# Kernel tuning notes

Hardware: AMD Instinct MI355X
Metric: run time of the kernel (lower is better)

The kernel has to match this reference:

```python
import jax, jax.numpy as jnp
import numpy as np
import math

H = 16        # num query heads
KV = 4        # num key/value heads
HD = 128      # head_dim
THETA = 10000.0

def _rope(x, cos, sin):
    # x: [B, h, S, HD]; cos/sin: [1, 1, S, HD//2]
    xr, xi = x[..., :HD // 2], x[..., HD // 2:]
    return jnp.concatenate([xr * cos - xi * sin, xr * sin + xi * cos], axis=-1)

def setup_inputs() -> dict:
    key = jax.random.key(0)
    ks = jax.random.split(key, 5)
    B, S, D = 1, 4096, 2048
    s = 1.0 / math.sqrt(D)
    return {
        "hidden_states": jax.random.normal(ks[0], (B, S, D), jnp.float32),
        "Wq": jax.random.normal(ks[1], (D, H * HD), jnp.float32) * s,
        "Wk": jax.random.normal(ks[2], (D, KV * HD), jnp.float32) * s,
        "Wv": jax.random.normal(ks[3], (D, KV * HD), jnp.float32) * s,
        "Wo": jax.random.normal(ks[4], (H * HD, D), jnp.float32) * s,
    }

def reference(hidden_states, Wq, Wk, Wv, Wo):
    B, S, D = hidden_states.shape
    # projections -> [B, h, S, HD]
    q = (hidden_states @ Wq).reshape(B, S, H, HD).transpose(0, 2, 1, 3)
    k = (hidden_states @ Wk).reshape(B, S, KV, HD).transpose(0, 2, 1, 3)
    v = (hidden_states @ Wv).reshape(B, S, KV, HD).transpose(0, 2, 1, 3)
    # rotary embedding (half-split layout, matching the torch module)
    inv_freq = 1.0 / (THETA ** (jnp.arange(0, HD, 2, dtype=jnp.float32) / HD))
    freqs = jnp.arange(S, dtype=jnp.float32)[:, None] * inv_freq[None, :]  # [S, HD//2]
    cos = jnp.cos(freqs)[None, None]
    sin = jnp.sin(freqs)[None, None]
    q = _rope(q, cos, sin)
    k = _rope(k, cos, sin)
    # GQA: repeat KV heads to match query heads
    rep = H // KV
    k = jnp.repeat(k, rep, axis=1)
    v = jnp.repeat(v, rep, axis=1)
    # non-causal scaled dot-product attention (world_size==1 path)
    scores = jnp.einsum('bhqd,bhkd->bhqk', q, k) / math.sqrt(HD)
    w = jax.nn.softmax(scores, axis=-1)
    o = jnp.einsum('bhqk,bhkd->bhqd', w, v)
    o = o.transpose(0, 2, 1, 3).reshape(B, S, H * HD)
    return o @ Wo
```

## Files before the change

kernel.cpp:

```cpp
#include <hip/hip_runtime.h>
#include <math.h>

#define S_LEN 4096
#define D_MODEL 2048
#define N_HEADS 16
#define N_KV 4
#define HEAD_DIM 128
#define KV_D 512
#define QKV_N 3072
#define SM_SHIFT 18.0f

typedef short bf16x8 __attribute__((ext_vector_type(8)));
typedef float f32x4 __attribute__((ext_vector_type(4)));

#if __has_builtin(__builtin_amdgcn_exp2f)
#define EXP2(x) __builtin_amdgcn_exp2f(x)
#else
#define EXP2(x) exp2f(x)
#endif

#define SBAR() asm volatile("s_barrier" ::: "memory")
#define VMCNT(n) asm volatile("s_waitcnt vmcnt(" #n ")" ::: "memory")

static __device__ __forceinline__ float b2f(unsigned short h) {
  return __uint_as_float(((unsigned int)h) << 16);
}
static __device__ __forceinline__ unsigned int cvt_pk_bf16(float a, float b) {
  unsigned int r;
  asm("v_cvt_pk_bf16_f32 %0, %1, %2" : "=v"(r) : "v"(a), "v"(b));
  return r;
}
static __device__ __forceinline__ unsigned short f2b(float f) {
  return (unsigned short)cvt_pk_bf16(f, f);
}

static __device__ __forceinline__ void gload_lds16(const unsigned short* g,
                                                   unsigned short* l) {
  __builtin_amdgcn_global_load_lds(
      (const __attribute__((address_space(1))) void*)g,
      (__attribute__((address_space(3))) void*)l, 16, 0, 0);
}

__global__ __launch_bounds__(256) void prep_kernel(
    const float* __restrict__ X, const float* __restrict__ Wq,
    const float* __restrict__ Wk, const float* __restrict__ Wv,
    const float* __restrict__ Wo, unsigned short* __restrict__ Xb,
    unsigned short* __restrict__ Wqkv, unsigned short* __restrict__ WoT) {
  __shared__ float tile[32][33];
  const int b = blockIdx.x, t = threadIdx.x;
  if (b < 4096) {
    int i = b * 2048 + t * 8;
    float4 a = *(const float4*)(X + i);
    float4 v = *(const float4*)(X + i + 4);
    unsigned int tmp[4] = {cvt_pk_bf16(a.x, a.y), cvt_pk_bf16(a.z, a.w),
                           cvt_pk_bf16(v.x, v.y), cvt_pk_bf16(v.z, v.w)};
    *(uint4*)&Xb[i] = *(uint4*)tmp;
    return;
  }
  int id = b - 4096;
  const float* src;
  unsigned short* dst;
  int N, tc, rowOff;
  if (id < 4096) { src = Wq; dst = Wqkv; N = 2048; tc = 64; rowOff = 0; }
  else if (id < 5120) { id -= 4096; src = Wk; dst = Wqkv; N = 512; tc = 16; rowOff = 2048; }
  else if (id < 6144) { id -= 5120; src = Wv; dst = Wqkv; N = 512; tc = 16; rowOff = 2560; }
  else { id -= 6144; src = Wo; dst = WoT; N = 2048; tc = 64; rowOff = 0; }
  const int c0 = (id % tc) * 32, r0 = (id / tc) * 32;
  const int col = t & 31, rb = t >> 5;
#pragma unroll
  for (int i = 0; i < 4; i++)
    tile[rb + i * 8][col] = src[(size_t)(r0 + rb + i * 8) * N + c0 + col];
  __syncthreads();
#pragma unroll
  for (int i = 0; i < 4; i++)
    dst[(size_t)(rowOff + c0 + rb + i * 8) * 2048 + r0 + col] =
        f2b(tile[col][rb + i * 8]);
}

__global__ __launch_bounds__(256) void bgemm_kernel(
    const unsigned short* __restrict__ A, const unsigned short* __restrict__ Bt,
    void* __restrict__ C, int M, int N, int K, int bf16_out) {
  __shared__ unsigned short As[128 * 32];
  __shared__ unsigned short Bs[128 * 32];

  const int t = threadIdx.x;
  const int w = t >> 6, l = t & 63;
  const int quad = l >> 4, lx = l & 15;
  const int row0 = blockIdx.y * 128, col0 = blockIdx.x * 128;
  const int wr = (w >> 1) * 64, wc = (w & 1) * 64;

  f32x4 acc[4][4];
#pragma unroll
  for (int mt = 0; mt < 4; mt++)
#pragma unroll
    for (int nt = 0; nt < 4; nt++) acc[mt][nt] = (f32x4){0.f, 0.f, 0.f, 0.f};

  for (int kt = 0; kt < K; kt += 32) {
    __syncthreads();
#pragma unroll
    for (int j = 0; j < 2; j++) {
      int ch = w * 128 + j * 64 + l;
      int r = ch >> 2, kc = (ch & 3) * 8;
      gload_lds16(A + (size_t)(row0 + r) * K + kt + kc, &As[ch * 8]);
      gload_lds16(Bt + (size_t)(col0 + r) * K + kt + kc, &Bs[ch * 8]);
    }
    __syncthreads();

    bf16x8 af[4], bfr[4];
#pragma unroll
    for (int mt = 0; mt < 4; mt++)
      af[mt] = *(const bf16x8*)&As[(wr + mt * 16 + lx) * 32 + quad * 8];
#pragma unroll
    for (int nt = 0; nt < 4; nt++)
      bfr[nt] = *(const bf16x8*)&Bs[(wc + nt * 16 + lx) * 32 + quad * 8];
#pragma unroll
    for (int mt = 0; mt < 4; mt++)
#pragma unroll
      for (int nt = 0; nt < 4; nt++)
        acc[mt][nt] = __builtin_amdgcn_mfma_f32_16x16x32_bf16(af[mt], bfr[nt],
                                                              acc[mt][nt], 0, 0, 0);
  }

  if (bf16_out) {
    unsigned short* Cp = (unsigned short*)C;
#pragma unroll
    for (int mt = 0; mt < 4; mt++)
#pragma unroll
      for (int nt = 0; nt < 4; nt++)
#pragma unroll
        for (int r = 0; r < 4; r++) {
          int row = row0 + wr + mt * 16 + quad * 4 + r;
          int col = col0 + wc + nt * 16 + lx;
          Cp[(size_t)row * N + col] = f2b(acc[mt][nt][r]);
        }
  } else {
    float* Cp = (float*)C;
#pragma unroll
    for (int mt = 0; mt < 4; mt++)
#pragma unroll
      for (int nt = 0; nt < 4; nt++)
#pragma unroll
        for (int r = 0; r < 4; r++) {
          int row = row0 + wr + mt * 16 + quad * 4 + r;
          int col = col0 + wc + nt * 16 + lx;
          Cp[(size_t)row * N + col] = acc[mt][nt][r];
        }
  }
}

__global__ __launch_bounds__(256) void ropev_kernel(
    unsigned short* __restrict__ QKV, unsigned short* __restrict__ Vt) {
  const int t = threadIdx.x;
  if (blockIdx.x < 20480) {
    int id = blockIdx.x * 256 + t;
    int d = id & 63;
    int rem = id >> 6;
    int head = rem % 20;
    int s = rem / 20;
    unsigned short* p;
    float scale;
    if (head < N_HEADS) {
      p = QKV + (size_t)s * QKV_N + head * HEAD_DIM;
      scale = 0.12753139187f;
    } else {
      p = QKV + (size_t)s * QKV_N + 2048 + (head - N_HEADS) * HEAD_DIM;
      scale = 1.0f;
    }
    float inv = exp2f(-(float)d * (13.287712379549449f / 64.0f));
    float ang = (float)s * inv;
    float sn, c;
    sincosf(ang, &sn, &c);
    float xr = b2f(p[d]), xi = b2f(p[d + 64]);
    p[d] = f2b((xr * c - xi * sn) * scale);
    p[d + 64] = f2b((xr * sn + xi * c) * scale);
    return;
  }
  __shared__ unsigned short tile[32][33];
  const unsigned short* Vb = QKV + 2560;
  int id = blockIdx.x - 20480;
  const int c0 = (id & 15) * 32;
  const int s0 = (id >> 4) * 32;
  const int col = t & 31, rbase = t >> 5;
#pragma unroll
  for (int i = 0; i < 4; i++) {
    int row = rbase + i * 8;
    tile[row][col] = Vb[(size_t)(s0 + row) * QKV_N + c0 + col];
  }
  __syncthreads();
#pragma unroll
  for (int i = 0; i < 4; i++) {
    int row = rbase + i * 8;
    Vt[(size_t)(c0 + row) * S_LEN + s0 + col] = tile[col][row];
  }
}

__global__ __launch_bounds__(256, 2) void attn_kernel(
    const unsigned short* __restrict__ Qb, const unsigned short* __restrict__ Kb,
    const unsigned short* __restrict__ Vt, unsigned short* __restrict__ Ob) {
  __shared__ unsigned short Ks[2][64 * 128];
  __shared__ unsigned short Vs[2][128 * 64];
  __shared__ unsigned short Pt[4][32 * 64];

  const int t = threadIdx.x;
  const int wave = t >> 6;
  const int lane = t & 63;
  const int quad = lane >> 4;
  const int lx = lane & 15;
  const int lx7 = lx & 7;
  const int qt = blockIdx.x;
  const int h = blockIdx.y;
  const int kvh = h >> 2;

  const unsigned short* Kg = Kb + kvh * HEAD_DIM;
  const unsigned short* Vg = Vt + (size_t)(kvh * HEAD_DIM) * S_LEN;

  const unsigned short* Qg =
      Qb + (size_t)(qt * 128 + wave * 32) * QKV_N + h * HEAD_DIM;
  bf16x8 qf[2][4];
#pragma unroll
  for (int qs = 0; qs < 2; qs++)
#pragma unroll
    for (int ks = 0; ks < 4; ks++)
      qf[qs][ks] = *(const bf16x8*)(Qg + (size_t)(qs * 16 + lx) * QKV_N +
                                    (quad << 3) + (ks << 5));

  f32x4 oacc[2][8];
#pragma unroll
  for (int qs = 0; qs < 2; qs++)
#pragma unroll
    for (int dt = 0; dt < 8; dt++) oacc[qs][dt] = (f32x4){0.f, 0.f, 0.f, 0.f};
  float l_st[2] = {0.f, 0.f};

  const unsigned short* kgp[4];
  const unsigned short* vgp[4];
#pragma unroll
  for (int j = 0; j < 4; j++) {
    int ch = (j * 4 + wave) * 64 + lane;
    int r = ch >> 4, c = ch & 15;
    kgp[j] = Kg + (size_t)r * QKV_N + ((c ^ (r & 7)) << 3);
    int d = ch >> 3, c2 = ch & 7;
    vgp[j] = Vg + (size_t)d * S_LEN + ((c2 ^ (d & 7)) << 3);
  }

  auto stage = [&](int kt, int b) {
#pragma unroll
    for (int j = 0; j < 4; j++) {
      int ch = (j * 4 + wave) * 64 + lane;
      gload_lds16(kgp[j] + (size_t)kt * (64 * QKV_N), &Ks[b][ch * 8]);
    }
#pragma unroll
    for (int j = 0; j < 4; j++) {
      int ch = (j * 4 + wave) * 64 + lane;
      gload_lds16(vgp[j] + kt * 64, &Vs[b][ch * 8]);
    }
  };

  stage(0, 0);

  for (int kt = 0; kt < S_LEN / 64; kt++) {
    VMCNT(4);
    SBAR();
    if (kt + 1 < S_LEN / 64) stage(kt + 1, (kt + 1) & 1);
    const unsigned short* KsC = Ks[kt & 1];
    const unsigned short* VsC = Vs[kt & 1];

#pragma unroll
    for (int ksub = 0; ksub < 4; ksub++) {
      bf16x8 kf[4];
#pragma unroll
      for (int ks = 0; ks < 4; ks++)
        kf[ks] = *(const bf16x8*)&KsC[(ksub * 16 + lx) * 128 +
                                      (((ks * 4 + quad) ^ lx7) << 3)];
#pragma unroll
      for (int qs = 0; qs < 2; qs++) {
        f32x4 a = (f32x4){-SM_SHIFT, -SM_SHIFT, -SM_SHIFT, -SM_SHIFT};
        __builtin_amdgcn_s_setprio(1);
#pragma unroll
        for (int ks = 0; ks < 4; ks++)
          a = __builtin_amdgcn_mfma_f32_16x16x32_bf16(kf[ks], qf[qs][ks], a, 0, 0, 0);
        __builtin_amdgcn_s_setprio(0);
        float p0 = EXP2(a[0]);
        float p1 = EXP2(a[1]);
        float p2 = EXP2(a[2]);
        float p3 = EXP2(a[3]);
        l_st[qs] += (p0 + p1) + (p2 + p3);
        *(uint2*)&Pt[wave][(qs * 16 + lx) * 64 +
                           (((2 * ksub + (quad >> 1)) ^ lx7) << 3) +
                           ((quad & 1) << 2)] =
            make_uint2(cvt_pk_bf16(p0, p1), cvt_pk_bf16(p2, p3));
      }
    }

    if (kt + 1 < S_LEN / 64) { VMCNT(8); } else { VMCNT(0); }
    SBAR();

#pragma unroll
    for (int st = 0; st < 2; st++) {
      const int pc = ((st * 4 + quad) ^ lx7) << 3;
      bf16x8 pb0 = *(const bf16x8*)&Pt[wave][lx * 64 + pc];
      bf16x8 pb1 = *(const bf16x8*)&Pt[wave][(16 + lx) * 64 + pc];
      __builtin_amdgcn_s_setprio(1);
#pragma unroll
      for (int dt = 0; dt < 8; dt++) {
        bf16x8 vf = *(const bf16x8*)&VsC[(dt * 16 + lx) * 64 + pc];
        oacc[0][dt] = __builtin_amdgcn_mfma_f32_16x16x32_bf16(vf, pb0, oacc[0][dt], 0, 0, 0);
        oacc[1][dt] = __builtin_amdgcn_mfma_f32_16x16x32_bf16(vf, pb1, oacc[1][dt], 0, 0, 0);
      }
      __builtin_amdgcn_s_setprio(0);
    }
  }

#pragma unroll
  for (int qs = 0; qs < 2; qs++) {
    float l = l_st[qs];
    l += __shfl_xor(l, 16);
    l += __shfl_xor(l, 32);
    float linv = 1.0f / l;
    unsigned short* ob = Ob +
        (size_t)(qt * 128 + wave * 32 + qs * 16 + lx) * D_MODEL + h * HEAD_DIM +
        quad * 4;
#pragma unroll
    for (int dt = 0; dt < 8; dt++) {
      *(uint2*)&ob[dt * 16] = make_uint2(
          cvt_pk_bf16(oacc[qs][dt][0] * linv, oacc[qs][dt][1] * linv),
          cvt_pk_bf16(oacc[qs][dt][2] * linv, oacc[qs][dt][3] * linv));
    }
  }
}

extern "C" void kernel_launch(void* const* d_in, const int* in_sizes, int n_in,
                              void* d_out, int out_size, void* d_ws,
                              size_t ws_size, hipStream_t stream) {
  const float* X = (const float*)d_in[0];
  const float* Wq = (const float*)d_in[1];
  const float* Wk = (const float*)d_in[2];
  const float* Wv = (const float*)d_in[3];
  const float* Wo = (const float*)d_in[4];
  float* out = (float*)d_out;

  const size_t MB = 1048576;
  char* ws = (char*)d_ws;
  unsigned short* Xb    = (unsigned short*)ws;
  unsigned short* WqkvT = (unsigned short*)(ws + 16 * MB);
  unsigned short* WoT   = (unsigned short*)(ws + 28 * MB);
  unsigned short* QKV   = (unsigned short*)(ws + 36 * MB);
  unsigned short* Vtr   = (unsigned short*)(ws + 60 * MB);
  unsigned short* Ob    = (unsigned short*)(ws + 64 * MB);

  dim3 blk(256);
  prep_kernel<<<14336, blk, 0, stream>>>(X, Wq, Wk, Wv, Wo, Xb, WqkvT, WoT);
  bgemm_kernel<<<dim3(QKV_N / 128, S_LEN / 128), blk, 0, stream>>>(
      Xb, WqkvT, QKV, S_LEN, QKV_N, D_MODEL, 1);
  ropev_kernel<<<20480 + 2048, blk, 0, stream>>>(QKV, Vtr);
  attn_kernel<<<dim3(S_LEN / 128, N_HEADS), blk, 0, stream>>>(
      QKV, QKV + 2048, Vtr, Ob);
  bgemm_kernel<<<dim3(D_MODEL / 128, S_LEN / 128), blk, 0, stream>>>(
      Ob, WoT, out, S_LEN, D_MODEL, D_MODEL, 0);
}
```

Baseline: 401.0 us.

## Replace projection GEMMs with 256-wide double-buffered swizzled-LDS MFMA kernel

Replaces the simple 128x128, BK=32, single-buffered GEMM with a templated 512-thread kernel. It uses 256x256 (QKV) or 128x256 (output) tiles with BK=64, double-buffered LDS staging via direct global-to-LDS loads, and XOR-swizzled LDS layout to avoid bank conflicts. It also adds phase-split MFMA issue with setprio. The aim is better data reuse, latency hiding and fewer LDS conflicts in the two projection GEMMs. In exchange it uses much more LDS and registers, lowering occupancy, and the QKV grid shrinks to 192 blocks, which may underfill the GPU.

```diff
diff --git a/kernel.cpp b/kernel.cpp
--- a/kernel.cpp
+++ b/kernel.cpp
@@ -77,72 +77,123 @@
         f2b(tile[col][rb + i * 8]);
 }
 
-__global__ __launch_bounds__(256) void bgemm_kernel(
+template <int BM, int BF16OUT>
+__global__ __launch_bounds__(512, 2) void gemm256_kernel(
     const unsigned short* __restrict__ A, const unsigned short* __restrict__ Bt,
-    void* __restrict__ C, int M, int N, int K, int bf16_out) {
-  __shared__ unsigned short As[128 * 32];
-  __shared__ unsigned short Bs[128 * 32];
+    void* __restrict__ C, int N, int K) {
+  constexpr int MT = BM / 32;
+  constexpr int ALT = BM / 64;
+  __shared__ unsigned short As[2][BM * 64];
+  __shared__ unsigned short Bs[2][256 * 64];
 
   const int t = threadIdx.x;
-  const int w = t >> 6, l = t & 63;
-  const int quad = l >> 4, lx = l & 15;
-  const int row0 = blockIdx.y * 128, col0 = blockIdx.x * 128;
-  const int wr = (w >> 1) * 64, wc = (w & 1) * 64;
-
-  f32x4 acc[4][4];
-#pragma unroll
-  for (int mt = 0; mt < 4; mt++)
+  const int w = t >> 6, lane = t & 63;
+  const int quad = lane >> 4, lx = lane & 15, lx7 = lx & 7;
+  const int wave_m = w >> 2, wave_n = w & 3;
+  const int row0 = blockIdx.y * BM, col0 = blockIdx.x * 256;
+
+  const unsigned short* agp[ALT];
+  const unsigned short* bgp[4];
+#pragma unroll
+  for (int j = 0; j < ALT; j++) {
+    int ch = j * 512 + t;
+    int r = ch >> 3, c = ch & 7;
+    agp[j] = A + (size_t)(row0 + r) * K + ((c ^ (r & 7)) << 3);
+  }
+#pragma unroll
+  for (int j = 0; j < 4; j++) {
+    int ch = j * 512 + t;
+    int r = ch >> 3, c = ch & 7;
+    bgp[j] = Bt + (size_t)(col0 + r) * K + ((c ^ (r & 7)) << 3);
+  }
+
+  auto stage = [&](int kt, int b) {
+#pragma unroll
+    for (int j = 0; j < ALT; j++)
+      gload_lds16(agp[j] + kt * 64, &As[b][(j * 512 + t) * 8]);
+#pragma unroll
+    for (int j = 0; j < 4; j++)
+      gload_lds16(bgp[j] + kt * 64, &Bs[b][(j * 512 + t) * 8]);
+  };
+
+  f32x4 acc[MT][4];
+#pragma unroll
+  for (int mt = 0; mt < MT; mt++)
 #pragma unroll
     for (int nt = 0; nt < 4; nt++) acc[mt][nt] = (f32x4){0.f, 0.f, 0.f, 0.f};
 
-  for (int kt = 0; kt < K; kt += 32) {
-    __syncthreads();
-#pragma unroll
-    for (int j = 0; j < 2; j++) {
-      int ch = w * 128 + j * 64 + l;
-      int r = ch >> 2, kc = (ch & 3) * 8;
-      gload_lds16(A + (size_t)(row0 + r) * K + kt + kc, &As[ch * 8]);
-      gload_lds16(Bt + (size_t)(col0 + r) * K + kt + kc, &Bs[ch * 8]);
-    }
-    __syncthreads();
-
-    bf16x8 af[4], bfr[4];
-#pragma unroll
-    for (int mt = 0; mt < 4; mt++)
-      af[mt] = *(const bf16x8*)&As[(wr + mt * 16 + lx) * 32 + quad * 8];
-#pragma unroll
-    for (int nt = 0; nt < 4; nt++)
-      bfr[nt] = *(const bf16x8*)&Bs[(wc + nt * 16 + lx) * 32 + quad * 8];
-#pragma unroll
-    for (int mt = 0; mt < 4; mt++)
+  const int NTK = K >> 6;
+  stage(0, 0);
+  stage(1, 1);
+
+  for (int kt = 0; kt < NTK; kt++) {
+    if (kt + 1 < NTK) {
+      if constexpr (BM == 256) { VMCNT(8); } else { VMCNT(6); }
+    } else {
+      VMCNT(0);
+    }
+    SBAR();
+    const unsigned short* AsC = As[kt & 1];
+    const unsigned short* BsC = Bs[kt & 1];
+
+#pragma unroll
+    for (int ph = 0; ph < 4; ph++) {
+      const int mq = ph >> 1, nq = ph & 1;
+      bf16x8 af[MT / 2][2], bf[2][2];
+#pragma unroll
+      for (int mt = 0; mt < MT / 2; mt++)
+#pragma unroll
+        for (int ks = 0; ks < 2; ks++)
+          af[mt][ks] = *(const bf16x8*)&AsC[
+              (wave_m * (MT * 16) + (mq * (MT / 2) + mt) * 16 + lx) * 64 +
+              (((ks * 4 + quad) ^ lx7) << 3)];
+#pragma unroll
+      for (int nt = 0; nt < 2; nt++)
+#pragma unroll
+        for (int ks = 0; ks < 2; ks++)
+          bf[nt][ks] = *(const bf16x8*)&BsC[
+              (wave_n * 64 + (nq * 2 + nt) * 16 + lx) * 64 +
+              (((ks * 4 + quad) ^ lx7) << 3)];
+      SBAR();
+      __builtin_amdgcn_s_setprio(1);
+#pragma unroll
+      for (int mt = 0; mt < MT / 2; mt++)
+#pragma unroll
+        for (int nt = 0; nt < 2; nt++)
+#pragma unroll
+          for (int ks = 0; ks < 2; ks++)
+            acc[mq * (MT / 2) + mt][nq * 2 + nt] =
+                __builtin_amdgcn_mfma_f32_16x16x32_bf16(
+                    af[mt][ks], bf[nt][ks], acc[mq * (MT / 2) + mt][nq * 2 + nt],
+                    0, 0, 0);
+      __builtin_amdgcn_s_setprio(0);
+      SBAR();
+    }
+    if (kt + 2 < NTK) stage(kt + 2, kt & 1);
+  }
+
+  if (BF16OUT) {
+    unsigned short* Cp = (unsigned short*)C;
+#pragma unroll
+    for (int mt = 0; mt < MT; mt++)
 #pragma unroll
       for (int nt = 0; nt < 4; nt++)
-        acc[mt][nt] = __builtin_amdgcn_mfma_f32_16x16x32_bf16(af[mt], bfr[nt],
-                                                              acc[mt][nt], 0, 0, 0);
-  }
-
-  if (bf16_out) {
-    unsigned short* Cp = (unsigned short*)C;
-#pragma unroll
-    for (int mt = 0; mt < 4; mt++)
-#pragma unroll
-      for (int nt = 0; nt < 4; nt++)
 #pragma unroll
         for (int r = 0; r < 4; r++) {
-          int row = row0 + wr + mt * 16 + quad * 4 + r;
-          int col = col0 + wc + nt * 16 + lx;
+          int row = row0 + wave_m * (MT * 16) + mt * 16 + quad * 4 + r;
+          int col = col0 + wave_n * 64 + nt * 16 + lx;
           Cp[(size_t)row * N + col] = f2b(acc[mt][nt][r]);
         }
   } else {
     float* Cp = (float*)C;
 #pragma unroll
-    for (int mt = 0; mt < 4; mt++)
+    for (int mt = 0; mt < MT; mt++)
 #pragma unroll
       for (int nt = 0; nt < 4; nt++)
 #pragma unroll
         for (int r = 0; r < 4; r++) {
-          int row = row0 + wr + mt * 16 + quad * 4 + r;
-          int col = col0 + wc + nt * 16 + lx;
+          int row = row0 + wave_m * (MT * 16) + mt * 16 + quad * 4 + r;
+          int col = col0 + wave_n * 64 + nt * 16 + lx;
           Cp[(size_t)row * N + col] = acc[mt][nt][r];
         }
   }
@@ -349,11 +400,11 @@
 
   dim3 blk(256);
   prep_kernel<<<14336, blk, 0, stream>>>(X, Wq, Wk, Wv, Wo, Xb, WqkvT, WoT);
-  bgemm_kernel<<<dim3(QKV_N / 128, S_LEN / 128), blk, 0, stream>>>(
-      Xb, WqkvT, QKV, S_LEN, QKV_N, D_MODEL, 1);
+  gemm256_kernel<256, 1><<<dim3(QKV_N / 256, S_LEN / 256), dim3(512), 0, stream>>>(
+      Xb, WqkvT, QKV, QKV_N, D_MODEL);
   ropev_kernel<<<20480 + 2048, blk, 0, stream>>>(QKV, Vtr);
   attn_kernel<<<dim3(S_LEN / 128, N_HEADS), blk, 0, stream>>>(
       QKV, QKV + 2048, Vtr, Ob);
-  bgemm_kernel<<<dim3(D_MODEL / 128, S_LEN / 128), blk, 0, stream>>>(
-      Ob, WoT, out, S_LEN, D_MODEL, D_MODEL, 0);
-}
+  gemm256_kernel<128, 0><<<dim3(D_MODEL / 256, S_LEN / 128), dim3(512), 0, stream>>>(
+      Ob, WoT, out, D_MODEL, D_MODEL);
+}
```

Result: slower. 410.8 us (+2.4%).
